# Performance work log

Hardware: AMD Instinct MI355X
Metric: run time of the kernel (lower is better)

Reference implementation:

```python
import jax, jax.numpy as jnp
import numpy as np

ALPHA, BETA, GAMMA = 1.0, 1.0, 0.7
WIN = 11
C1 = 0.01 ** 2
C2 = 0.03 ** 2


def get_sobel_kernels(n1=1, n2=2, n3=2):
    a = np.asarray
    Sx = a([[[-n1, 0, n1], [-n2, 0, n2], [-n1, 0, n1]],
            [[-n2, 0, n2], [-n3 * n2, 0, n3 * n2], [-n2, 0, n2]],
            [[-n1, 0, n1], [-n2, 0, n2], [-n1, 0, n1]]])
    Sy = a([[[-n1, -n2, -n1], [0, 0, 0], [n1, n2, n1]],
            [[-n2, -n3 * n2, -n2], [0, 0, 0], [n2, n3 * n2, n2]],
            [[-n1, -n2, -n1], [0, 0, 0], [n1, n2, n1]]])
    Sz = a([[[-n1, -n2, -n1], [-n2, -n3 * n2, -n2], [-n1, -n2, -n1]],
            [[0, 0, 0], [0, 0, 0], [0, 0, 0]],
            [[n1, n2, n1], [n2, n3 * n2, n2], [n1, n2, n1]]])
    Sd11 = a([[[0, n1, n2], [-n1, 0, n1], [-n2, -n1, 0]],
              [[0, n2, n2 * n3], [-n2, 0, n2], [-n2 * n3, -n2, 0]],
              [[0, n1, n2], [-n1, 0, n1], [-n2, -n1, 0]]])
    Sd12 = a([[[-n2, -n1, 0], [-n1, 0, n1], [0, n1, n2]],
              [[-n2 * n3, -n2, 0], [-n2, 0, n2], [0, n2, n2 * n3]],
              [[-n2, -n1, 0], [-n1, 0, n1], [0, n1, n2]]])
    Sd21 = Sd11.T
    Sd22 = Sd12.T
    Sd31 = a([-S.T for S in Sd11.T])
    Sd32 = a([S.T for S in Sd12.T])
    return np.stack([Sx, Sy, Sz, Sd11, Sd12, Sd21, Sd22, Sd31, Sd32]).astype(np.float32)

# (9,1,3,3,3) fused sobel bank -- single grouped conv instead of 9 launches
SOBEL_W = jnp.asarray(get_sobel_kernels()[:, None])


def _gauss1d():
    g = jnp.exp(-(jnp.arange(WIN, dtype=jnp.float32) - WIN // 2) ** 2 / (2 * 1.5 ** 2))
    return g / g.sum()

G1D = _gauss1d()


def conv3d(x, w):
    return jax.lax.conv_general_dilated(
        x, w, window_strides=(1, 1, 1), padding='SAME',
        dimension_numbers=('NCDHW', 'OIDHW', 'NCDHW'))


def gauss_filter(x):
    # separable 11-tap gaussian along D, H, W (== full 11^3 window, zero-padded SAME)
    x = conv3d(x, G1D.reshape(1, 1, WIN, 1, 1))
    x = conv3d(x, G1D.reshape(1, 1, 1, WIN, 1))
    x = conv3d(x, G1D.reshape(1, 1, 1, 1, WIN))
    return x


def edge_map(img):
    # GradEdge3D.__call__ with a=1, C=1
    B, C, D, H, W = img.shape
    xp = jnp.pad(img, ((0, 0), (0, 0), (1, 1), (1, 1), (1, 1)), mode='reflect')
    g = conv3d(xp, SOBEL_W)                       # (B, 9, D+2, H+2, W+2)
    gm = jnp.sqrt(jnp.sum((g + 1e-6) ** 2 + 1e-6, axis=1))  # (B, D+2, H+2, W+2)
    gm = gm[:, 1:-1, 1:-1, 1:-1]
    norm = (gm - gm.min()) / (gm.max() - gm.min() + 1e-6)
    return norm.reshape(B, 1, D, H, W)


def ssim_value(pred, target):
    mu_p = gauss_filter(pred)
    mu_t = gauss_filter(target)
    mu_p2, mu_t2, mu_pt = mu_p ** 2, mu_t ** 2, mu_p * mu_t
    sig_p = gauss_filter(pred * pred) - mu_p2
    sig_t = gauss_filter(target * target) - mu_t2
    sig_pt = gauss_filter(pred * target) - mu_pt
    ssim_map = ((2 * mu_pt + C1) * (2 * sig_pt + C2)) / ((mu_p2 + mu_t2 + C1) * (sig_p + sig_t + C2))
    return 1.0 - ssim_map.mean()


def setup_inputs() -> dict:
    key = jax.random.key(0)
    k1, k2 = jax.random.split(key)
    shape = (2, 1, 128, 128, 128)
    return {
        'pred': jax.random.uniform(k1, shape, dtype=jnp.float32),
        'target': jax.random.uniform(k2, shape, dtype=jnp.float32),
    }


def reference(pred, target):
    loss_mse = jnp.mean((pred - target) ** 2)
    loss_ssim = ssim_value(pred, target)
    # GMELoss3D: lam_errors=[(1.0, L1Loss())], reduction='sum'
    loss_gme = 1e-6 + jnp.mean(jnp.abs(edge_map(pred) - edge_map(target)))
    total = ALPHA * loss_mse + BETA * loss_ssim + GAMMA * loss_gme
    return (total, loss_mse, loss_ssim, loss_gme)
```

## Files before the change

kernel.cpp:

```cpp
#include <hip/hip_runtime.h>


#define VOL 4194304
#define HV  2097152

typedef _Float16 h2 __attribute__((ext_vector_type(2)));
typedef _Float16 h8 __attribute__((ext_vector_type(8)));

constexpr float GW[11] = {
    0.00102838f, 0.00759876f, 0.03600077f, 0.10936070f, 0.21300554f,
    0.26601173f,
    0.21300554f, 0.10936070f, 0.03600077f, 0.00759876f, 0.00102838f};


__device__ __forceinline__ void wblur_body(
    const float* __restrict__ p, const float* __restrict__ t,
    _Float16* __restrict__ A, double* __restrict__ mseB, const int bidx) {
  __shared__ float sr[2][138];
  __shared__ float dr[2][138];
  __shared__ float redw[256];
  const int tid = threadIdx.x;
  const int rl = tid >> 7;
  const int x  = tid & 127;
  const int rowBase = bidx << 4;
  if (x < 5)    { sr[rl][x] = 0.f;      dr[rl][x] = 0.f; }
  if (x >= 123) { sr[rl][10 + x] = 0.f; dr[rl][10 + x] = 0.f; }
  float pv = p[((rowBase + rl) << 7) + x];
  float tv = t[((rowBase + rl) << 7) + x];
  float msel = 0.f;
  for (int it = 0; it < 8; ++it) {
    const int row  = rowBase + (it << 1) + rl;
    const int base = row << 7;
    const float sv = pv + tv;
    const float dv = pv - tv;
    sr[rl][5 + x] = sv; dr[rl][5 + x] = dv;
    msel += dv * dv;
    __syncthreads();
    float pvN = 0.f, tvN = 0.f;
    if (it < 7) {
      const int baseN = (row + 2) << 7;
      pvN = p[baseN + x]; tvN = t[baseN + x];
    }
    float as = 0.f, ad = 0.f, ass = 0.f, add_ = 0.f;
#pragma unroll
    for (int k = 0; k < 11; ++k) {
      const float w = GW[k];
      const float a = sr[rl][x + k];
      const float b = dr[rl][x + k];
      const float wa = w * a;
      const float wb = w * b;
      as += wa; ad += wb;
      ass += wa * a; add_ += wb * b;
    }
    const int idx = base + x;
    A[idx]           = (_Float16)as;
    A[VOL + idx]     = (_Float16)ad;
    A[2 * VOL + idx] = (_Float16)ass;
    A[3 * VOL + idx] = (_Float16)add_;
    __syncthreads();
    pv = pvN; tv = tvN;
  }
  redw[tid] = msel;
  __syncthreads();
  for (int s = 128; s > 0; s >>= 1) {
    if (tid < s) redw[tid] += redw[tid + s];
    __syncthreads();
  }
  if (tid == 0) atomicAdd(&mseB[(bidx & 63) << 3], (double)redw[0]);
}

__device__ __forceinline__ void sobel_body(
    const float* __restrict__ p, const float* __restrict__ t,
    _Float16* __restrict__ gmP, _Float16* __restrict__ gmT,
    unsigned int* __restrict__ ui, const int bx, const int by, const int bz) {
  __shared__ float sb[1296];
  __shared__ float rmin[256];
  __shared__ float rmax[256];
  const int tid = threadIdx.x;
  const int tx = tid & 15;
  const int ty = tid >> 4;
  const int x0 = bx << 4;
  const int y0 = by << 4;
  const int vol = bz >> 4;
  const int b   = (bz >> 3) & 1;
  const int z0  = (bz & 7) << 4;
  const float* __restrict__ img = vol ? t : p;
  _Float16* __restrict__ gm = vol ? gmT : gmP;
  const int vb = b << 21;

  const int ly1 = tid / 24, lx1 = tid % 24;
  const bool v1 = (lx1 < 18);
  int gy1 = y0 - 1 + ly1; gy1 = gy1 < 0 ? 1 : (gy1 > 127 ? 126 : gy1);
  int gx1 = x0 - 1 + lx1; gx1 = gx1 < 0 ? 1 : (gx1 > 127 ? 126 : gx1);
  const int off1 = (gy1 << 7) + gx1;
  const int s2i = tid + 256;
  const int ly2 = s2i / 24, lx2 = s2i % 24;
  const bool v2 = (s2i < 432) && (lx2 < 18);
  int gy2 = y0 - 1 + ly2; gy2 = gy2 < 0 ? 1 : (gy2 > 127 ? 126 : gy2);
  int gx2 = x0 - 1 + lx2; gx2 = gx2 < 0 ? 1 : (gx2 > 127 ? 126 : gx2);
  const int off2 = (gy2 << 7) + gx2;
  const int rb = ty * 24 + tx;
  const int gbase = vb + (z0 << 14) + ((y0 + ty) << 7) + (x0 + tx);

  float Y0[7], Y1[7], Y2[7];
  float rv1 = 0.f, rv2 = 0.f;
  float lmin = 3.4e38f, lmax = 0.f;

#define LOADR(ZS) {                                                         \
    const int zc_ = (ZS) > 127 ? 126 : (ZS);                                \
    const int za_ = vb + (zc_ << 14);                                       \
    if (v1) rv1 = img[za_ + off1];                                          \
    if (v2) rv2 = img[za_ + off2]; }

#define WRITELDS(BOFF) {                                                    \
    if (v1) sb[(BOFF) + tid] = rv1;                                         \
    if (v2) sb[(BOFF) + s2i] = rv2; }

#define COMPY(P) {                                                          \
    const int o_ = (P) * 432 + rb;                                          \
    const float r00 = sb[o_],      r01 = sb[o_ + 1],  r02 = sb[o_ + 2];     \
    const float r10 = sb[o_ + 24], r11 = sb[o_ + 25], r12 = sb[o_ + 26];    \
    const float r20 = sb[o_ + 48], r21 = sb[o_ + 49], r22 = sb[o_ + 50];    \
    const float dx0 = r02 - r00, dx1 = r12 - r10, dx2 = r22 - r20;          \
    const float ux0 = r00 + r01 + r02, ux1 = r10 + r11 + r12,               \
                ux2 = r20 + r21 + r22;                                      \
    const float sx0 = ux0 + r01, sx1 = ux1 + r11, sx2 = ux2 + r21;          \
    Y##P[1] = dx0 + dx1 + dx2;                                    \
    Y##P[0] = Y##P[1] + dx1;                                      \
    Y##P[2] = sx2 - sx0;                                          \
    Y##P[4] = sx0 + sx1 + sx2;                                    \
    Y##P[3] = Y##P[4] + sx1;                                      \
    Y##P[5] = ux2 - ux0;                                          \
    Y##P[6] = (ux0 + ux2) + 2.f * ux1; }

#define EMIT(I, P0, P1, P2) {                                               \
    const float E_ = Y##P0[0] + Y##P1[0] + Y##P2[0];                        \
    const float g1 = E_ + Y##P1[0];                                         \
    const float tA = Y##P0[1] + Y##P1[1] + Y##P2[1];                        \
    const float A_ = tA + Y##P1[1];                                         \
    const float D_ = Y##P0[2] + Y##P1[2] + Y##P2[2];                        \
    const float g2 = D_ + Y##P1[2];                                         \
    const float g3 = Y##P2[3] - Y##P0[3];                                   \
    const float C_ = Y##P2[4] - Y##P0[4];                                   \
    const float B_ = (Y##P0[5] + Y##P2[5]) + 2.f * Y##P1[5];                \
    const float F_ = Y##P2[6] - Y##P0[6];                                   \
    const float g4 = A_ - B_, g5 = A_ + B_;                                 \
    const float g6 = C_ - D_, g7 = C_ + D_;                                 \
    const float g8 = E_ - F_, g9 = E_ + F_;                                 \
    float ss_ = 9e-6f, t_;                                                  \
    t_ = g1 + 1e-6f; ss_ = fmaf(t_, t_, ss_);                               \
    t_ = g2 + 1e-6f; ss_ = fmaf(t_, t_, ss_);                               \
    t_ = g3 + 1e-6f; ss_ = fmaf(t_, t_, ss_);                               \
    t_ = g4 + 1e-6f; ss_ = fmaf(t_, t_, ss_);                               \
    t_ = g5 + 1e-6f; ss_ = fmaf(t_, t_, ss_);                               \
    t_ = g6 + 1e-6f; ss_ = fmaf(t_, t_, ss_);                               \
    t_ = g7 + 1e-6f; ss_ = fmaf(t_, t_, ss_);                               \
    t_ = g8 + 1e-6f; ss_ = fmaf(t_, t_, ss_);                               \
    t_ = g9 + 1e-6f; ss_ = fmaf(t_, t_, ss_);                               \
    const _Float16 gh = (_Float16)sqrtf(ss_);                               \
    gm[gbase + ((I) << 14)] = gh;                                           \
    const float gq = (float)gh;                                             \
    lmin = fminf(lmin, gq); lmax = fmaxf(lmax, gq); }

#define BODY(I, P0, P1, P2) {                                               \
    WRITELDS((P2) * 432);                                                   \
    LOADR(z0 + (I) + 2);                                                    \
    __syncthreads();                                                        \
    COMPY(P2);                                                              \
    EMIT(I, P0, P1, P2); }

  {
    const int zp = (z0 == 0) ? 1 : (z0 - 1);
    LOADR(zp);  WRITELDS(0);
    LOADR(z0);  WRITELDS(432);
    __syncthreads();
    COMPY(0);
    COMPY(1);
    LOADR(z0 + 1);
  }
  for (int ii = 0; ii < 15; ii += 3) {
    BODY(ii,     0, 1, 2);
    BODY(ii + 1, 1, 2, 0);
    BODY(ii + 2, 2, 0, 1);
  }
  BODY(15, 0, 1, 2);

#undef BODY
#undef EMIT
#undef COMPY
#undef WRITELDS
#undef LOADR

  rmin[tid] = lmin; rmax[tid] = lmax;
  __syncthreads();
  for (int st = 128; st > 0; st >>= 1) {
    if (tid < st) {
      rmin[tid] = fminf(rmin[tid], rmin[tid + st]);
      rmax[tid] = fmaxf(rmax[tid], rmax[tid + st]);
    }
    __syncthreads();
  }
  if (tid == 0) {
    const int bin = (bx + (by << 3) + (bz << 6)) & 63;
    atomicMax(&ui[vol * 1024 + (bin << 4)], ~__float_as_uint(rmin[0]));
    atomicMax(&ui[2048 + vol * 1024 + (bin << 4)], __float_as_uint(rmax[0]));
  }
}

__device__ __forceinline__ void blury_body(
    const _Float16* __restrict__ A, _Float16* __restrict__ B,
    const int z, const int yseg, const int batch) {
  __shared__ h8 s[4][26][16];
  const int tid = threadIdx.x;
  const int y0 = yseg << 4;
  const int b8 = batch << 18;
  const h8* __restrict__ Ah = (const h8*)A;
  h8* __restrict__ Bh = (h8*)B;
  const int slice8 = b8 + (z << 11);
  for (int q = 0; q < 4; ++q) {
    const h8* __restrict__ Aq = Ah + (q << 19) + slice8;
    for (int l = tid; l < 416; l += 256) {
      const int row = l >> 4, xc = l & 15;
      const int y = y0 - 5 + row;
      h8 v{};
      if ((unsigned)y < 128u) v = Aq[(y << 4) + xc];
      s[q][row][xc] = v;
    }
  }
  __syncthreads();
  const int xc = tid & 15;
  const int yo = tid >> 4;
  const int wbase = slice8 + ((y0 + yo) << 4) + xc;
#pragma unroll
  for (int q = 0; q < 4; ++q) {
    h8 acc{};
#pragma unroll
    for (int k = 0; k < 11; ++k) {
      const _Float16 w = (_Float16)GW[k];
      acc += w * s[q][yo + k][xc];
    }
    Bh[(q << 19) + wbase] = acc;
  }
}

__device__ __forceinline__ void edge_body(
    const _Float16* __restrict__ gmP, const _Float16* __restrict__ gmT,
    const unsigned int* __restrict__ ui, double* __restrict__ absB,
    const int bidx) {
  __shared__ float rede[256];
  unsigned umnp = 0u, umnt = 0u, umxp = 0u, umxt = 0u;
  for (int j = 0; j < 64; ++j) {
    const unsigned a0 = ui[j << 4];
    const unsigned a1 = ui[1024 + (j << 4)];
    const unsigned a2 = ui[2048 + (j << 4)];
    const unsigned a3 = ui[3072 + (j << 4)];
    umnp = umnp > a0 ? umnp : a0;
    umnt = umnt > a1 ? umnt : a1;
    umxp = umxp > a2 ? umxp : a2;
    umxt = umxt > a3 ? umxt : a3;
  }
  const float mnp = __uint_as_float(~umnp);
  const float mnt = __uint_as_float(~umnt);
  const float mxp = __uint_as_float(umxp);
  const float mxt = __uint_as_float(umxt);
  const float scp = 1.f / (mxp - mnp + 1e-6f);
  const float sct = 1.f / (mxt - mnt + 1e-6f);
  const h8* __restrict__ gp = (const h8*)gmP;
  const h8* __restrict__ gt = (const h8*)gmT;
  float lsum = 0.f;
  const int base = bidx << 9;
#pragma unroll
  for (int i = 0; i < 2; ++i) {
    const int idx = base + (i << 8) + threadIdx.x;
    const h8 a = gp[idx];
    const h8 b = gt[idx];
#pragma unroll
    for (int j = 0; j < 8; ++j)
      lsum += fabsf(((float)a[j] - mnp) * scp - ((float)b[j] - mnt) * sct);
  }
  rede[threadIdx.x] = lsum;
  __syncthreads();
  for (int s = 128; s > 0; s >>= 1) {
    if (threadIdx.x < s) rede[threadIdx.x] += rede[threadIdx.x + s];
    __syncthreads();
  }
  if (threadIdx.x == 0)
    atomicAdd(&absB[(bidx & 63) << 3], (double)rede[0]);
}

__global__ __launch_bounds__(256) void k_fused_a(
    const float* __restrict__ p, const float* __restrict__ t,
    _Float16* __restrict__ A, double* __restrict__ mseB,
    _Float16* __restrict__ gmP, _Float16* __restrict__ gmT,
    unsigned int* __restrict__ ui) {
  const int bid = blockIdx.x;
  if ((bid & 1) == 0) {
    wblur_body(p, t, A, mseB, bid >> 1);
  } else {
    const int s = bid >> 1;
    sobel_body(p, t, gmP, gmT, ui, s & 7, (s >> 3) & 7, s >> 6);
  }
}

__global__ __launch_bounds__(256) void k_fused_b(
    const _Float16* __restrict__ A, _Float16* __restrict__ B,
    const _Float16* __restrict__ gmP, const _Float16* __restrict__ gmT,
    const unsigned int* __restrict__ ui, double* __restrict__ absB) {
  const int bid = blockIdx.x;
  const int r3 = bid % 3;
  if (r3 < 2) {
    const int idx = (bid / 3) * 2 + r3;
    blury_body(A, B, idx & 127, (idx >> 7) & 7, idx >> 10);
  } else {
    edge_body(gmP, gmT, ui, absB, bid / 3);
  }
}

__global__ __launch_bounds__(256) void k_zblur_ssim(
    const _Float16* __restrict__ B, double* __restrict__ ssimB) {
  __shared__ h8 s[4][26][16];
  __shared__ float red[256];
  const int tid = threadIdx.x;
  const int y  = blockIdx.x;
  const int z0 = blockIdx.y << 4;
  const int b8 = blockIdx.z << 18;
  const h8* __restrict__ Bh = (const h8*)B;
  const int col8 = b8 + (y << 4);
  for (int q = 0; q < 4; ++q) {
    const h8* __restrict__ Bq = Bh + (q << 19) + col8;
    for (int l = tid; l < 416; l += 256) {
      const int row = l >> 4, xc = l & 15;
      const int zz = z0 - 5 + row;
      h8 v{};
      if ((unsigned)zz < 128u) v = Bq[(zz << 11) + xc];
      s[q][row][xc] = v;
    }
  }
  __syncthreads();
  const int xc = tid & 15;
  const int zo = tid >> 4;
  h8 m[4];
#pragma unroll
  for (int q = 0; q < 4; ++q) {
    h8 acc{};
#pragma unroll
    for (int k = 0; k < 11; ++k) {
      const _Float16 w = (_Float16)GW[k];
      acc += w * s[q][zo + k][xc];
    }
    m[q] = acc;
  }
  float lsum = 0.f;
#pragma unroll
  for (int j = 0; j < 8; ++j) {
    const float mus = (float)m[0][j];
    const float mud = (float)m[1][j];
    const float ess = (float)m[2][j];
    const float edd = (float)m[3][j];
    const float S2 = mus * mus, D2 = mud * mud;
    const float num = ((S2 - D2) * 0.5f + 1e-4f) *
                      ((ess - edd - S2 + D2) * 0.5f + 9e-4f);
    const float den = ((S2 + D2) * 0.5f + 1e-4f) *
                      ((ess + edd - S2 - D2) * 0.5f + 9e-4f);
    lsum += num / den;
  }
  red[tid] = lsum;
  __syncthreads();
  for (int st = 128; st > 0; st >>= 1) {
    if (tid < st) red[tid] += red[tid + st];
    __syncthreads();
  }
  if (tid == 0) {
    const int bin = (blockIdx.x + (blockIdx.y << 3) + blockIdx.z) & 63;
    atomicAdd(&ssimB[bin << 3], (double)red[0]);
  }
}

__global__ void k_final(const double* __restrict__ dbl, float* __restrict__ out) {
  if (threadIdx.x == 0 && blockIdx.x == 0) {
    double ms = 0.0, ss = 0.0, ab = 0.0;
    for (int j = 0; j < 64; ++j) {
      ms += dbl[j << 3];
      ss += dbl[512 + (j << 3)];
      ab += dbl[1024 + (j << 3)];
    }
    const double N = 4194304.0;
    const double mse   = ms / N;
    const double ssiml = 1.0 - ss / N;
    const double gme   = 1e-6 + ab / N;
    const double total = mse + ssiml + 0.7 * gme;
    out[0] = (float)total;
    out[1] = (float)mse;
    out[2] = (float)ssiml;
    out[3] = (float)gme;
  }
}

extern "C" void kernel_launch(void* const* d_in, const int* in_sizes, int n_in,
                              void* d_out, int out_size, void* d_ws, size_t ws_size,
                              hipStream_t stream) {
  const float* p = (const float*)d_in[0];
  const float* t = (const float*)d_in[1];
  _Float16* A = (_Float16*)d_ws;
  _Float16* B = A + (size_t)4 * VOL;
  char* accb = (char*)d_ws + (size_t)20 * VOL;
  double* dbl = (double*)accb;
  unsigned int* ui = (unsigned int*)(accb + 12288);
  _Float16* gmP = (_Float16*)((char*)d_ws + 88080384);
  _Float16* gmT = gmP + VOL;
  float* out = (float*)d_out;

  hipMemsetAsync(accb, 0, 28672, stream);
  k_fused_a<<<4096, 256, 0, stream>>>(p, t, A, dbl, gmP, gmT, ui);
  k_fused_b<<<3072, 256, 0, stream>>>(A, B, gmP, gmT, ui, dbl + 1024);
  k_zblur_ssim<<<dim3(128, 8, 2), 256, 0, stream>>>(B, dbl + 512);
  k_final<<<1, 64, 0, stream>>>(dbl, out);
}
```

Measured before the change: 153.4 us.

## Interleave four blur channels per voxel and lengthen sobel z-runs

The intermediate blur buffers now hold the four channels (sum, diff, sum², diff²) interleaved per voxel instead of in four separate planes. The x-blur writes one 8-byte vector per voxel, and the y/z blur kernels read and write contiguous 64-wide h8 rows, which are meant to give wider, fully coalesced accesses. Separately, each sobel block now walks 32 z-slices instead of 16, halving the sobel block count and cutting the redundant halo-slice loads. The fused-A grid is rebalanced to two wblur blocks per sobel block. The cost is less parallelism and longer serial work per sobel block.

```diff
diff --git a/kernel.cpp b/kernel.cpp
--- a/kernel.cpp
+++ b/kernel.cpp
@@ -5,12 +5,14 @@
 #define HV  2097152
 
 typedef _Float16 h2 __attribute__((ext_vector_type(2)));
+typedef _Float16 h4 __attribute__((ext_vector_type(4)));
 typedef _Float16 h8 __attribute__((ext_vector_type(8)));
 
 constexpr float GW[11] = {
     0.00102838f, 0.00759876f, 0.03600077f, 0.10936070f, 0.21300554f,
     0.26601173f,
     0.21300554f, 0.10936070f, 0.03600077f, 0.00759876f, 0.00102838f};
+
 
 
 __device__ __forceinline__ void wblur_body(
@@ -28,6 +30,7 @@
   float pv = p[((rowBase + rl) << 7) + x];
   float tv = t[((rowBase + rl) << 7) + x];
   float msel = 0.f;
+  h4* __restrict__ A4 = (h4*)A;
   for (int it = 0; it < 8; ++it) {
     const int row  = rowBase + (it << 1) + rl;
     const int base = row << 7;
@@ -52,11 +55,10 @@
       as += wa; ad += wb;
       ass += wa * a; add_ += wb * b;
     }
-    const int idx = base + x;
-    A[idx]           = (_Float16)as;
-    A[VOL + idx]     = (_Float16)ad;
-    A[2 * VOL + idx] = (_Float16)ass;
-    A[3 * VOL + idx] = (_Float16)add_;
+    h4 o;
+    o[0] = (_Float16)as;  o[1] = (_Float16)ad;
+    o[2] = (_Float16)ass; o[3] = (_Float16)add_;
+    A4[base + x] = o;
     __syncthreads();
     pv = pvN; tv = tvN;
   }
@@ -81,9 +83,9 @@
   const int ty = tid >> 4;
   const int x0 = bx << 4;
   const int y0 = by << 4;
-  const int vol = bz >> 4;
-  const int b   = (bz >> 3) & 1;
-  const int z0  = (bz & 7) << 4;
+  const int vol = bz >> 3;
+  const int b   = (bz >> 2) & 1;
+  const int z0  = (bz & 3) << 5;
   const float* __restrict__ img = vol ? t : p;
   _Float16* __restrict__ gm = vol ? gmT : gmP;
   const int vb = b << 21;
@@ -178,12 +180,13 @@
     COMPY(1);
     LOADR(z0 + 1);
   }
-  for (int ii = 0; ii < 15; ii += 3) {
+  for (int ii = 0; ii < 30; ii += 3) {
     BODY(ii,     0, 1, 2);
     BODY(ii + 1, 1, 2, 0);
     BODY(ii + 2, 2, 0, 1);
   }
-  BODY(15, 0, 1, 2);
+  BODY(30, 0, 1, 2);
+  BODY(31, 1, 2, 0);
 
 #undef BODY
 #undef EMIT
@@ -210,36 +213,32 @@
 __device__ __forceinline__ void blury_body(
     const _Float16* __restrict__ A, _Float16* __restrict__ B,
     const int z, const int yseg, const int batch) {
-  __shared__ h8 s[4][26][16];
+  __shared__ h8 s[26][64];
   const int tid = threadIdx.x;
   const int y0 = yseg << 4;
-  const int b8 = batch << 18;
   const h8* __restrict__ Ah = (const h8*)A;
   h8* __restrict__ Bh = (h8*)B;
-  const int slice8 = b8 + (z << 11);
-  for (int q = 0; q < 4; ++q) {
-    const h8* __restrict__ Aq = Ah + (q << 19) + slice8;
-    for (int l = tid; l < 416; l += 256) {
-      const int row = l >> 4, xc = l & 15;
-      const int y = y0 - 5 + row;
-      h8 v{};
-      if ((unsigned)y < 128u) v = Aq[(y << 4) + xc];
-      s[q][row][xc] = v;
-    }
-  }
-  __syncthreads();
-  const int xc = tid & 15;
-  const int yo = tid >> 4;
-  const int wbase = slice8 + ((y0 + yo) << 4) + xc;
-#pragma unroll
-  for (int q = 0; q < 4; ++q) {
+  const int slice8 = (batch << 20) + (z << 13);
+  for (int l = tid; l < 1664; l += 256) {
+    const int row = l >> 6, xc = l & 63;
+    const int y = y0 - 5 + row;
+    h8 v{};
+    if ((unsigned)y < 128u) v = Ah[slice8 + (y << 6) + xc];
+    s[row][xc] = v;
+  }
+  __syncthreads();
+  const int xc = tid & 63;
+  const int yg = tid >> 6;
+#pragma unroll
+  for (int r = 0; r < 4; ++r) {
+    const int yo = (yg << 2) + r;
     h8 acc{};
 #pragma unroll
     for (int k = 0; k < 11; ++k) {
       const _Float16 w = (_Float16)GW[k];
-      acc += w * s[q][yo + k][xc];
-    }
-    Bh[(q << 19) + wbase] = acc;
+      acc += w * s[yo + k][xc];
+    }
+    Bh[slice8 + ((y0 + yo) << 6) + xc] = acc;
   }
 }
 
@@ -294,10 +293,11 @@
     _Float16* __restrict__ gmP, _Float16* __restrict__ gmT,
     unsigned int* __restrict__ ui) {
   const int bid = blockIdx.x;
-  if ((bid & 1) == 0) {
-    wblur_body(p, t, A, mseB, bid >> 1);
+  const int r3 = bid % 3;
+  if (r3 < 2) {
+    wblur_body(p, t, A, mseB, (bid / 3) * 2 + r3);
   } else {
-    const int s = bid >> 1;
+    const int s = bid / 3;
     sobel_body(p, t, gmP, gmT, ui, s & 7, (s >> 3) & 7, s >> 6);
   }
 }
@@ -318,51 +318,46 @@
 
 __global__ __launch_bounds__(256) void k_zblur_ssim(
     const _Float16* __restrict__ B, double* __restrict__ ssimB) {
-  __shared__ h8 s[4][26][16];
+  __shared__ h8 s[26][64];
   __shared__ float red[256];
   const int tid = threadIdx.x;
   const int y  = blockIdx.x;
   const int z0 = blockIdx.y << 4;
-  const int b8 = blockIdx.z << 18;
   const h8* __restrict__ Bh = (const h8*)B;
-  const int col8 = b8 + (y << 4);
-  for (int q = 0; q < 4; ++q) {
-    const h8* __restrict__ Bq = Bh + (q << 19) + col8;
-    for (int l = tid; l < 416; l += 256) {
-      const int row = l >> 4, xc = l & 15;
-      const int zz = z0 - 5 + row;
-      h8 v{};
-      if ((unsigned)zz < 128u) v = Bq[(zz << 11) + xc];
-      s[q][row][xc] = v;
-    }
-  }
-  __syncthreads();
-  const int xc = tid & 15;
-  const int zo = tid >> 4;
-  h8 m[4];
-#pragma unroll
-  for (int q = 0; q < 4; ++q) {
-    h8 acc{};
+  const int col8 = (blockIdx.z << 20) + (y << 6);
+  for (int l = tid; l < 1664; l += 256) {
+    const int row = l >> 6, xc = l & 63;
+    const int zz = z0 - 5 + row;
+    h8 v{};
+    if ((unsigned)zz < 128u) v = Bh[col8 + (zz << 13) + xc];
+    s[row][xc] = v;
+  }
+  __syncthreads();
+  const int xc = tid & 63;
+  const int zg = tid >> 6;
+  float lsum = 0.f;
+#pragma unroll
+  for (int r = 0; r < 4; ++r) {
+    const int zo = (zg << 2) + r;
+    h8 m{};
 #pragma unroll
     for (int k = 0; k < 11; ++k) {
       const _Float16 w = (_Float16)GW[k];
-      acc += w * s[q][zo + k][xc];
-    }
-    m[q] = acc;
-  }
-  float lsum = 0.f;
-#pragma unroll
-  for (int j = 0; j < 8; ++j) {
-    const float mus = (float)m[0][j];
-    const float mud = (float)m[1][j];
-    const float ess = (float)m[2][j];
-    const float edd = (float)m[3][j];
-    const float S2 = mus * mus, D2 = mud * mud;
-    const float num = ((S2 - D2) * 0.5f + 1e-4f) *
-                      ((ess - edd - S2 + D2) * 0.5f + 9e-4f);
-    const float den = ((S2 + D2) * 0.5f + 1e-4f) *
-                      ((ess + edd - S2 - D2) * 0.5f + 9e-4f);
-    lsum += num / den;
+      m += w * s[zo + k][xc];
+    }
+#pragma unroll
+    for (int j = 0; j < 2; ++j) {
+      const float mus = (float)m[4 * j + 0];
+      const float mud = (float)m[4 * j + 1];
+      const float ess = (float)m[4 * j + 2];
+      const float edd = (float)m[4 * j + 3];
+      const float S2 = mus * mus, D2 = mud * mud;
+      const float num = ((S2 - D2) * 0.5f + 1e-4f) *
+                        ((ess - edd - S2 + D2) * 0.5f + 9e-4f);
+      const float den = ((S2 + D2) * 0.5f + 1e-4f) *
+                        ((ess + edd - S2 - D2) * 0.5f + 9e-4f);
+      lsum += num / den;
+    }
   }
   red[tid] = lsum;
   __syncthreads();
@@ -411,7 +406,7 @@
   float* out = (float*)d_out;
 
   hipMemsetAsync(accb, 0, 28672, stream);
-  k_fused_a<<<4096, 256, 0, stream>>>(p, t, A, dbl, gmP, gmT, ui);
+  k_fused_a<<<3072, 256, 0, stream>>>(p, t, A, dbl, gmP, gmT, ui);
   k_fused_b<<<3072, 256, 0, stream>>>(A, B, gmP, gmT, ui, dbl + 1024);
   k_zblur_ssim<<<dim3(128, 8, 2), 256, 0, stream>>>(B, dbl + 512);
   k_final<<<1, 64, 0, stream>>>(dbl, out);
```

After: 150.7 us. No clear change (-1.8%).
